# Kernel tuning notes

Hardware: AMD Instinct MI355X
Metric: run time of the kernel (lower is better)

## Reference

```python
import jax, jax.numpy as jnp
import numpy as np

N = 50000      # nodes
E = 800000     # edges
IN = 128       # in_dim
H = 128        # hidden_dim
OUT = 64       # out_dim
B = 6          # block_num
NEG_SLOPE = 0.01  # nn.LeakyReLU default


def setup_inputs() -> dict:
    key = jax.random.key(0)
    ks = jax.random.split(key, 10)
    s = 0.05
    return {
        "inputs": jax.random.normal(ks[0], (N, IN), jnp.float32),
        "edges": jax.random.randint(ks[1], (2, E), 0, N, jnp.int32),
        "w_in": jax.random.normal(ks[2], (IN, H), jnp.float32) * s,
        "b_in": jnp.zeros((H,), jnp.float32),
        "w1": jax.random.normal(ks[3], (B, H, H), jnp.float32) * s,
        "b1": jnp.zeros((B, H), jnp.float32),
        "w2": jax.random.normal(ks[4], (B, H, H), jnp.float32) * s,
        "b2": jnp.zeros((B, H), jnp.float32),
        "w_out": jax.random.normal(ks[5], (H, OUT), jnp.float32) * s,
        "b_out": jnp.zeros((OUT,), jnp.float32),
    }


def _leaky(x):
    return jnp.where(x >= 0, x, NEG_SLOPE * x)


def _gcn_conv(x, W, b, src, dst, norm):
    # GCNConv: out = D^{-1/2}(A+I)D^{-1/2} (x W) + b, with self-loops folded in.
    xw = x @ W                                   # [N, d_out]
    msg = xw[src] * norm[src, None]              # gather + edge scaling [E, d_out]
    agg = jax.ops.segment_sum(msg, dst, num_segments=N)
    agg = agg * norm[:, None] + xw * (norm * norm)[:, None]  # neighbors + self-loop
    return agg + b


def reference(inputs, edges, w_in, b_in, w1, b1, w2, b2, w_out, b_out):
    src, dst = edges[0], edges[1]
    deg = 1.0 + jax.ops.segment_sum(jnp.ones((E,), inputs.dtype), dst, num_segments=N)
    norm = jax.lax.rsqrt(deg)                    # [N]

    x = _leaky(_gcn_conv(inputs, w_in, b_in, src, dst, norm))
    for i in range(B):  # fixed small layer loop (structurally distinct params)
        h = _leaky(_gcn_conv(x, w1[i], b1[i], src, dst, norm))
        h = _leaky(_gcn_conv(h, w2[i], b2[i], src, dst, norm))
        x = (x + h) * 0.5
    # dropout in eval mode -> identity
    x_out = _gcn_conv(x, w_out, b_out, src, dst, norm)
    return (x_out, x)
```

## Files before the change

kernel.cpp:

```cpp
#include <hip/hip_runtime.h>

#define NNODES 50000
#define NPAD   50048
#define NEDGES 800000
#define HDIM 128
#define OUTDIM 64

#define GEMM_GRID 196
#define GEMM_BLK  512
#define GEMM_WAVES (GEMM_GRID * (GEMM_BLK / 64))
#define GEMM_TILES (NPAD / 16)

typedef short short8 __attribute__((ext_vector_type(8)));
typedef _Float16 half8 __attribute__((ext_vector_type(8)));
typedef _Float16 half4 __attribute__((ext_vector_type(4)));
typedef float f32x4 __attribute__((ext_vector_type(4)));

__device__ __forceinline__ unsigned short f2bf(float f) {
    unsigned int u = __builtin_bit_cast(unsigned int, f);
    unsigned int r = (u + 0x7FFFu + ((u >> 16) & 1u)) >> 16;
    return (unsigned short)r;
}
__device__ __forceinline__ float bf2f(unsigned short b) {
    unsigned int u = ((unsigned int)b) << 16;
    return __builtin_bit_cast(float, u);
}

__global__ void count_kernel(const int* __restrict__ dst, int* __restrict__ deg,
                             int* __restrict__ epos) {
    int e = blockIdx.x * 256 + threadIdx.x;
    if (e < NEDGES) epos[e] = atomicAdd(&deg[dst[e]], 1);
}

__global__ __launch_bounds__(256) void bsum_kernel(const int* __restrict__ deg,
                                                   int* __restrict__ bsum) {
    __shared__ int red[256];
    int i = blockIdx.x * 256 + threadIdx.x;
    red[threadIdx.x] = (i < NNODES) ? deg[i] : 0;
    __syncthreads();
    for (int off = 128; off; off >>= 1) {
        if (threadIdx.x < off) red[threadIdx.x] += red[threadIdx.x + off];
        __syncthreads();
    }
    if (threadIdx.x == 0) bsum[blockIdx.x] = red[0];
}

__global__ __launch_bounds__(256) void bscan_kernel(const int* __restrict__ bsum,
                                                    int* __restrict__ bofs) {
    __shared__ int s[256];
    int t = threadIdx.x;
    int v = (t < 196) ? bsum[t] : 0;
    s[t] = v;
    __syncthreads();
    for (int off = 1; off < 256; off <<= 1) {
        int u = (t >= off) ? s[t - off] : 0;
        __syncthreads();
        s[t] += u;
        __syncthreads();
    }
    if (t < 196) bofs[t] = s[t] - v;
}

__global__ __launch_bounds__(256) void emit_kernel(
    const int* __restrict__ deg, const int* __restrict__ bofs,
    int* __restrict__ row_ptr, float* __restrict__ norm) {
    __shared__ int s[256];
    int t = threadIdx.x;
    int i = blockIdx.x * 256 + t;
    int v = (i < NNODES) ? deg[i] : 0;
    s[t] = v;
    __syncthreads();
    for (int off = 1; off < 256; off <<= 1) {
        int u = (t >= off) ? s[t - off] : 0;
        __syncthreads();
        s[t] += u;
        __syncthreads();
    }
    int excl = s[t] - v + bofs[blockIdx.x];
    if (i < NNODES) {
        row_ptr[i] = excl;
        norm[i] = rsqrtf(1.0f + (float)v);
    }
    if (i == NNODES - 1) row_ptr[NNODES] = NEDGES;
}

__global__ void fill_kernel(const int* __restrict__ src, const int* __restrict__ dst,
                            const int* __restrict__ epos, const int* __restrict__ row_ptr,
                            int* __restrict__ sorted_src) {
    int e = blockIdx.x * 256 + threadIdx.x;
    if (e < NEDGES) sorted_src[row_ptr[dst[e]] + epos[e]] = src[e];
}

__global__ __launch_bounds__(256) void prep_w_kernel(
    const float* __restrict__ w_in, const float* __restrict__ w1,
    const float* __restrict__ w2, const float* __restrict__ w_out,
    unsigned short* __restrict__ wT, _Float16* __restrict__ w2f) {
    int idx = blockIdx.x * 256 + threadIdx.x;
    if (idx < 16384 + 98304) {
        const float* W;
        unsigned short* o;
        int e;
        if (idx < 16384) {
            W = w_in; o = wT; e = idx;
        } else {
            int j = idx - 16384; int m = j >> 14; e = j & 16383;
            W = w1 + ((size_t)m << 14); o = wT + (size_t)(1 + m) * 32768;
        }
        int k = e >> 7, n = e & 127;
        float v = W[e];
        unsigned short h = f2bf(v);
        o[(size_t)n * 256 + k] = h;
        o[(size_t)n * 256 + 128 + k] = f2bf(v - bf2f(h));
    } else if (idx < 16384 + 196608) {
        int j = idx - 16384 - 98304; int m = j >> 14; int e = j & 16383;
        int k = e >> 7, n = e & 127;
        w2f[(size_t)m * 16384 + n * 128 + k] = (_Float16)w2[((size_t)m << 14) + e];
    } else {
        int e = idx - 212992;
        int k = e >> 6, n = e & 63;
        float v = w_out[e];
        unsigned short h = f2bf(v);
        unsigned short* o = wT + (size_t)7 * 32768;
        o[(size_t)n * 256 + k] = h;
        o[(size_t)n * 256 + 128 + k] = f2bf(v - bf2f(h));
    }
}

__global__ __launch_bounds__(256) void split_x_kernel(
    const float* __restrict__ x, unsigned short* __restrict__ xc) {
    int gid = blockIdx.x * 256 + threadIdx.x;
    int row = gid >> 6;
    int kk = (gid & 63) * 2;
    float2 v = {0.f, 0.f};
    if (row < NNODES) v = *(const float2*)(x + (size_t)row * 128 + kk);
    unsigned short h0 = f2bf(v.x), h1 = f2bf(v.y);
    unsigned short l0 = f2bf(v.x - bf2f(h0)), l1 = f2bf(v.y - bf2f(h1));
    *(unsigned int*)(xc + (size_t)row * 256 + kk) =
        (unsigned int)h0 | ((unsigned int)h1 << 16);
    *(unsigned int*)(xc + (size_t)row * 256 + 128 + kk) =
        (unsigned int)l0 | ((unsigned int)l1 << 16);
}

template <int NCOLS>
__global__ __launch_bounds__(GEMM_BLK) void gemm_bf_kernel(
    const unsigned short* __restrict__ xc, const unsigned short* __restrict__ wT,
    const float* __restrict__ norm, _Float16* __restrict__ y) {
    __shared__ unsigned short Blds[NCOLS * 256];
    const int t = threadIdx.x;
    const int wave = t >> 6, lane = t & 63, quad = lane >> 4, l16 = lane & 15;

    constexpr int NCH = NCOLS * 32;
#pragma unroll
    for (int i = 0; i < NCH / GEMM_BLK; ++i) {
        int C = i * GEMM_BLK + t;
        int n = C >> 5, c = C & 31;
        const unsigned short* gp = wT + ((size_t)n << 8) + ((c ^ (n & 7)) << 3);
        unsigned short* lp = Blds + ((size_t)C << 3);
        __builtin_amdgcn_global_load_lds(
            (const __attribute__((address_space(1))) void*)gp,
            (__attribute__((address_space(3))) void*)lp, 16, 0, 0);
    }
    __syncthreads();

    const int wid = blockIdx.x * (GEMM_BLK / 64) + wave;
    const int sw = l16 & 7;
    const bool has1 = (wid + GEMM_WAVES) < GEMM_TILES;
    const int rb0 = wid * 16;
    const int rb1 = has1 ? (wid + GEMM_WAVES) * 16 : 0;

    short8 a0[8], a1[8];
    const unsigned short* ap0 = xc + ((size_t)(rb0 + l16) << 8) + quad * 8;
    const unsigned short* ap1 = xc + ((size_t)(rb1 + l16) << 8) + quad * 8;
#pragma unroll
    for (int ck = 0; ck < 8; ++ck) a0[ck] = *(const short8*)(ap0 + ck * 32);
#pragma unroll
    for (int ck = 0; ck < 8; ++ck) a1[ck] = *(const short8*)(ap1 + ck * 32);

    float nm0[4], nm1[4];
#pragma unroll
    for (int r = 0; r < 4; ++r) {
        int r0 = rb0 + quad * 4 + r;
        int r1 = rb1 + quad * 4 + r;
        nm0[r] = norm[r0 < NNODES ? r0 : 0];
        nm1[r] = norm[r1 < NNODES ? r1 : 0];
    }

#pragma unroll
    for (int nt = 0; nt < NCOLS / 16; ++nt) {
        const unsigned short* bp = Blds + ((size_t)(nt * 16 + l16) << 8);
        short8 bh[4], bl[4];
#pragma unroll
        for (int ck = 0; ck < 4; ++ck) {
            bh[ck] = *(const short8*)(bp + (((ck * 4 + quad) ^ sw) << 3));
            bl[ck] = *(const short8*)(bp + (((16 + ck * 4 + quad) ^ sw) << 3));
        }
        f32x4 ac0 = (f32x4){0.f, 0.f, 0.f, 0.f};
        f32x4 ac1 = (f32x4){0.f, 0.f, 0.f, 0.f};
#pragma unroll
        for (int ck = 0; ck < 4; ++ck) {
            ac0 = __builtin_amdgcn_mfma_f32_16x16x32_bf16(a0[ck], bh[ck], ac0, 0, 0, 0);
            ac1 = __builtin_amdgcn_mfma_f32_16x16x32_bf16(a1[ck], bh[ck], ac1, 0, 0, 0);
            ac0 = __builtin_amdgcn_mfma_f32_16x16x32_bf16(a0[ck], bl[ck], ac0, 0, 0, 0);
            ac1 = __builtin_amdgcn_mfma_f32_16x16x32_bf16(a1[ck], bl[ck], ac1, 0, 0, 0);
            ac0 = __builtin_amdgcn_mfma_f32_16x16x32_bf16(a0[4 + ck], bh[ck], ac0, 0, 0, 0);
            ac1 = __builtin_amdgcn_mfma_f32_16x16x32_bf16(a1[4 + ck], bh[ck], ac1, 0, 0, 0);
        }
        int col = nt * 16 + l16;
#pragma unroll
        for (int r = 0; r < 4; ++r) {
            int r0 = rb0 + quad * 4 + r;
            if (r0 < NNODES) y[(size_t)r0 * NCOLS + col] = (_Float16)(ac0[r] * nm0[r]);
            int r1 = rb1 + quad * 4 + r;
            if (has1 && r1 < NNODES) y[(size_t)r1 * NCOLS + col] = (_Float16)(ac1[r] * nm1[r]);
        }
    }
}

__global__ __launch_bounds__(GEMM_BLK) void gemm_f16_kernel(
    const _Float16* __restrict__ A, const _Float16* __restrict__ wf,
    const float* __restrict__ norm, _Float16* __restrict__ y) {
    __shared__ _Float16 Blds[128 * 128];
    const int t = threadIdx.x;
    const int wave = t >> 6, lane = t & 63, quad = lane >> 4, l16 = lane & 15;

#pragma unroll
    for (int i = 0; i < 2048 / GEMM_BLK; ++i) {
        int C = i * GEMM_BLK + t;
        int n = C >> 4, c = C & 15;
        const _Float16* gp = wf + ((size_t)n << 7) + ((c ^ (n & 7)) << 3);
        _Float16* lp = Blds + ((size_t)C << 3);
        __builtin_amdgcn_global_load_lds(
            (const __attribute__((address_space(1))) void*)gp,
            (__attribute__((address_space(3))) void*)lp, 16, 0, 0);
    }
    __syncthreads();

    const int wid = blockIdx.x * (GEMM_BLK / 64) + wave;
    const int sw = l16 & 7;
    const bool has1 = (wid + GEMM_WAVES) < GEMM_TILES;
    const int rb0 = wid * 16;
    const int rb1 = has1 ? (wid + GEMM_WAVES) * 16 : 0;

    half8 a0[4], a1[4];
    const _Float16* ap0 = A + ((size_t)(rb0 + l16) << 7) + quad * 8;
    const _Float16* ap1 = A + ((size_t)(rb1 + l16) << 7) + quad * 8;
#pragma unroll
    for (int ck = 0; ck < 4; ++ck) a0[ck] = *(const half8*)(ap0 + ck * 32);
#pragma unroll
    for (int ck = 0; ck < 4; ++ck) a1[ck] = *(const half8*)(ap1 + ck * 32);

    float nm0[4], nm1[4];
#pragma unroll
    for (int r = 0; r < 4; ++r) {
        int r0 = rb0 + quad * 4 + r;
        int r1 = rb1 + quad * 4 + r;
        nm0[r] = norm[r0 < NNODES ? r0 : 0];
        nm1[r] = norm[r1 < NNODES ? r1 : 0];
    }

#pragma unroll
    for (int nt = 0; nt < 8; ++nt) {
        const _Float16* bp = Blds + ((size_t)(nt * 16 + l16) << 7);
        half8 b[4];
#pragma unroll
        for (int ck = 0; ck < 4; ++ck)
            b[ck] = *(const half8*)(bp + (((ck * 4 + quad) ^ sw) << 3));
        f32x4 ac0 = (f32x4){0.f, 0.f, 0.f, 0.f};
        f32x4 ac1 = (f32x4){0.f, 0.f, 0.f, 0.f};
#pragma unroll
        for (int ck = 0; ck < 4; ++ck) {
            ac0 = __builtin_amdgcn_mfma_f32_16x16x32_f16(a0[ck], b[ck], ac0, 0, 0, 0);
            ac1 = __builtin_amdgcn_mfma_f32_16x16x32_f16(a1[ck], b[ck], ac1, 0, 0, 0);
        }
        int col = nt * 16 + l16;
#pragma unroll
        for (int r = 0; r < 4; ++r) {
            int r0 = rb0 + quad * 4 + r;
            if (r0 < NNODES) y[(size_t)r0 * 128 + col] = (_Float16)(ac0[r] * nm0[r]);
            int r1 = rb1 + quad * 4 + r;
            if (has1 && r1 < NNODES) y[(size_t)r1 * 128 + col] = (_Float16)(ac1[r] * nm1[r]);
        }
    }
}

template <int MODE, bool WOUT, bool OUT16>
__global__ __launch_bounds__(256) void gather_fin128(
    const _Float16* __restrict__ y, const int* __restrict__ row_ptr,
    const int* __restrict__ sorted_src, const float* __restrict__ norm,
    const float* __restrict__ bias, const unsigned short* __restrict__ xcres,
    float* __restrict__ out, unsigned short* __restrict__ xcout,
    _Float16* __restrict__ h16) {
    const int wave = threadIdx.x >> 6;
    const int lane = threadIdx.x & 63;
    const int g = lane >> 4, j = lane & 15;
    const int n = blockIdx.x * 16 + wave * 4 + g;
    const int beg = row_ptr[n];
    const int deg = row_ptr[n + 1] - beg;
    int dmax = deg;
    dmax = max(dmax, __shfl_xor(dmax, 16));
    dmax = max(dmax, __shfl_xor(dmax, 32));

    float acc[8];
#pragma unroll
    for (int c = 0; c < 8; ++c) acc[c] = 0.f;

    for (int i = 0; i < dmax; i += 8) {
        int sarr[8];
#pragma unroll
        for (int u = 0; u < 8; ++u)
            sarr[u] = (i + u < deg) ? sorted_src[beg + i + u] : -1;
        half8 h[8];
#pragma unroll
        for (int u = 0; u < 8; ++u)
            if (sarr[u] >= 0)
                h[u] = *(const half8*)(y + ((size_t)sarr[u] << 7) + j * 8);
#pragma unroll
        for (int u = 0; u < 8; ++u)
            if (sarr[u] >= 0) {
#pragma unroll
                for (int c = 0; c < 8; ++c) acc[c] += (float)h[u][c];
            }
    }

    const half8 sh = *(const half8*)(y + ((size_t)n << 7) + j * 8);
    const float4 b0 = *(const float4*)(bias + j * 8);
    const float4 b1 = *(const float4*)(bias + j * 8 + 4);
    const float bb[8] = {b0.x, b0.y, b0.z, b0.w, b1.x, b1.y, b1.z, b1.w};
    const float nm = norm[n];
    float v[8];
#pragma unroll
    for (int c = 0; c < 8; ++c) {
        float t = (acc[c] + (float)sh[c]) * nm + bb[c];
        v[c] = t >= 0.f ? t : 0.01f * t;
    }
    if (MODE == 1) {
        short8 hw = *(const short8*)(xcres + ((size_t)n << 8) + j * 8);
        short8 lw = *(const short8*)(xcres + ((size_t)n << 8) + 128 + j * 8);
#pragma unroll
        for (int c = 0; c < 8; ++c) {
            float xr = bf2f((unsigned short)hw[c]) + bf2f((unsigned short)lw[c]);
            v[c] = (xr + v[c]) * 0.5f;
        }
    }
    if (WOUT) {
        float4 o0 = {v[0], v[1], v[2], v[3]};
        float4 o1 = {v[4], v[5], v[6], v[7]};
        *(float4*)(out + ((size_t)n << 7) + j * 8) = o0;
        *(float4*)(out + ((size_t)n << 7) + j * 8 + 4) = o1;
    }
    if (OUT16) {
        half8 o;
#pragma unroll
        for (int c = 0; c < 8; ++c) o[c] = (_Float16)v[c];
        *(half8*)(h16 + ((size_t)n << 7) + j * 8) = o;
    } else {
        short8 hi, lo;
#pragma unroll
        for (int c = 0; c < 8; ++c) {
            unsigned short hv = f2bf(v[c]);
            hi[c] = (short)hv;
            lo[c] = (short)f2bf(v[c] - bf2f(hv));
        }
        *(short8*)(xcout + ((size_t)n << 8) + j * 8) = hi;
        *(short8*)(xcout + ((size_t)n << 8) + 128 + j * 8) = lo;
    }
}

__global__ __launch_bounds__(256) void gather_fin64(
    const _Float16* __restrict__ y, const int* __restrict__ row_ptr,
    const int* __restrict__ sorted_src, const float* __restrict__ norm,
    const float* __restrict__ bias, float* __restrict__ out) {
    const int wave = threadIdx.x >> 6;
    const int lane = threadIdx.x & 63;
    const int g = lane >> 4, j = lane & 15;
    const int n = blockIdx.x * 16 + wave * 4 + g;
    const int beg = row_ptr[n];
    const int deg = row_ptr[n + 1] - beg;
    int dmax = deg;
    dmax = max(dmax, __shfl_xor(dmax, 16));
    dmax = max(dmax, __shfl_xor(dmax, 32));

    float acc[4] = {0.f, 0.f, 0.f, 0.f};
    for (int i = 0; i < dmax; i += 8) {
        int sarr[8];
#pragma unroll
        for (int u = 0; u < 8; ++u)
            sarr[u] = (i + u < deg) ? sorted_src[beg + i + u] : -1;
        half4 h[8];
#pragma unroll
        for (int u = 0; u < 8; ++u)
            if (sarr[u] >= 0)
                h[u] = *(const half4*)(y + ((size_t)sarr[u] << 6) + j * 4);
#pragma unroll
        for (int u = 0; u < 8; ++u)
            if (sarr[u] >= 0) {
#pragma unroll
                for (int c = 0; c < 4; ++c) acc[c] += (float)h[u][c];
            }
    }

    const half4 sh = *(const half4*)(y + ((size_t)n << 6) + j * 4);
    const float4 b = *(const float4*)(bias + j * 4);
    const float bb[4] = {b.x, b.y, b.z, b.w};
    const float nm = norm[n];
    float4 o;
    o.x = (acc[0] + (float)sh[0]) * nm + bb[0];
    o.y = (acc[1] + (float)sh[1]) * nm + bb[1];
    o.z = (acc[2] + (float)sh[2]) * nm + bb[2];
    o.w = (acc[3] + (float)sh[3]) * nm + bb[3];
    *(float4*)(out + ((size_t)n << 6) + j * 4) = o;
}

extern "C" void kernel_launch(void* const* d_in, const int* in_sizes, int n_in,
                              void* d_out, int out_size, void* d_ws, size_t ws_size,
                              hipStream_t stream) {
    const float* inputs = (const float*)d_in[0];
    const int* edges = (const int*)d_in[1];
    const int* src = edges;
    const int* dst = edges + NEDGES;
    const float* w_in  = (const float*)d_in[2];
    const float* b_in  = (const float*)d_in[3];
    const float* w1    = (const float*)d_in[4];
    const float* b1    = (const float*)d_in[5];
    const float* w2    = (const float*)d_in[6];
    const float* b2    = (const float*)d_in[7];
    const float* w_out = (const float*)d_in[8];
    const float* b_out = (const float*)d_in[9];

    float* out  = (float*)d_out;
    float* xout = out;
    float* x    = out + (size_t)NNODES * OUTDIM;

    char* p = (char*)d_ws;
    auto alloc = [&](size_t bytes) {
        char* r = p;
        p += (bytes + 63) & ~(size_t)63;
        return r;
    };
    int* deg        = (int*)alloc(NNODES * 4);
    int* epos       = (int*)alloc(NEDGES * 4);
    int* row_ptr    = (int*)alloc((NNODES + 1) * 4);
    int* bsum       = (int*)alloc(256 * 4);
    int* bofs       = (int*)alloc(256 * 4);
    int* sorted_src = (int*)alloc(NEDGES * 4);
    float* normb    = (float*)alloc(NNODES * 4);
    unsigned short* wT = (unsigned short*)alloc((size_t)245760 * 2);
    _Float16* w2f   = (_Float16*)alloc((size_t)6 * 16384 * 2);
    unsigned short* xc_x = (unsigned short*)alloc((size_t)NPAD * 256 * 2);
    unsigned short* xc_in = (unsigned short*)alloc((size_t)NPAD * 256 * 2);
    _Float16* h16   = (_Float16*)alloc((size_t)NPAD * 128 * 2);
    _Float16* y     = (_Float16*)alloc((size_t)NNODES * HDIM * 2);

    hipMemsetAsync(deg, 0, NNODES * sizeof(int), stream);
    count_kernel<<<(NEDGES + 255) / 256, 256, 0, stream>>>(dst, deg, epos);
    bsum_kernel<<<196, 256, 0, stream>>>(deg, bsum);
    bscan_kernel<<<1, 256, 0, stream>>>(bsum, bofs);
    emit_kernel<<<196, 256, 0, stream>>>(deg, bofs, row_ptr, normb);
    fill_kernel<<<(NEDGES + 255) / 256, 256, 0, stream>>>(src, dst, epos, row_ptr, sorted_src);
    prep_w_kernel<<<864, 256, 0, stream>>>(w_in, w1, w2, w_out, wT, w2f);

    split_x_kernel<<<(NPAD * 64) / 256, 256, 0, stream>>>(inputs, xc_in);
    gemm_bf_kernel<128><<<GEMM_GRID, GEMM_BLK, 0, stream>>>(xc_in, wT, normb, y);
    gather_fin128<0, false, false><<<NNODES / 16, 256, 0, stream>>>(
        y, row_ptr, sorted_src, normb, b_in, nullptr, nullptr, xc_x, nullptr);

    for (int i = 0; i < 6; ++i) {
        gemm_bf_kernel<128><<<GEMM_GRID, GEMM_BLK, 0, stream>>>(
            xc_x, wT + (size_t)(1 + i) * 32768, normb, y);
        gather_fin128<0, false, true><<<NNODES / 16, 256, 0, stream>>>(
            y, row_ptr, sorted_src, normb, b1 + i * HDIM, nullptr, nullptr, nullptr, h16);
        gemm_f16_kernel<<<GEMM_GRID, GEMM_BLK, 0, stream>>>(
            h16, w2f + (size_t)i * 16384, normb, y);
        if (i < 5)
            gather_fin128<1, false, false><<<NNODES / 16, 256, 0, stream>>>(
                y, row_ptr, sorted_src, normb, b2 + i * HDIM, xc_x, nullptr, xc_x, nullptr);
        else
            gather_fin128<1, true, false><<<NNODES / 16, 256, 0, stream>>>(
                y, row_ptr, sorted_src, normb, b2 + i * HDIM, xc_x, x, xc_x, nullptr);
    }

    gemm_bf_kernel<64><<<GEMM_GRID, GEMM_BLK, 0, stream>>>(
        xc_x, wT + (size_t)7 * 32768, normb, y);
    gather_fin64<<<NNODES / 16, 256, 0, stream>>>(
        y, row_ptr, sorted_src, normb, b_out, xout);
}
```

Before: 788.1 us.

## Sort nodes by degree for gathers and use one row tile per GEMM wave

New measurement: 1.207 ms. 1.53x slower.

```diff
diff --git a/kernel.cpp b/kernel.cpp
--- a/kernel.cpp
+++ b/kernel.cpp
@@ -6,15 +6,17 @@
 #define HDIM 128
 #define OUTDIM 64
 
-#define GEMM_GRID 196
+#define GEMM_GRID 391
 #define GEMM_BLK  512
-#define GEMM_WAVES (GEMM_GRID * (GEMM_BLK / 64))
 #define GEMM_TILES (NPAD / 16)
+
+#define DBUCKETS 512
 
 typedef short short8 __attribute__((ext_vector_type(8)));
 typedef _Float16 half8 __attribute__((ext_vector_type(8)));
 typedef _Float16 half4 __attribute__((ext_vector_type(4)));
 typedef float f32x4 __attribute__((ext_vector_type(4)));
+typedef float f32x8 __attribute__((ext_vector_type(8)));
 
 __device__ __forceinline__ unsigned short f2bf(float f) {
     unsigned int u = __builtin_bit_cast(unsigned int, f);
@@ -89,6 +91,37 @@
                             int* __restrict__ sorted_src) {
     int e = blockIdx.x * 256 + threadIdx.x;
     if (e < NEDGES) sorted_src[row_ptr[dst[e]] + epos[e]] = src[e];
+}
+
+__global__ void dhist_kernel(const int* __restrict__ deg, int* __restrict__ dcount) {
+    int i = blockIdx.x * 256 + threadIdx.x;
+    if (i < NNODES) atomicAdd(&dcount[min(deg[i], DBUCKETS - 1)], 1);
+}
+
+__global__ __launch_bounds__(DBUCKETS) void dscan_kernel(const int* __restrict__ dcount,
+                                                         int* __restrict__ dofs) {
+    __shared__ int s[DBUCKETS];
+    int t = threadIdx.x;
+    int v = dcount[t];
+    s[t] = v;
+    __syncthreads();
+    for (int off = 1; off < DBUCKETS; off <<= 1) {
+        int u = (t >= off) ? s[t - off] : 0;
+        __syncthreads();
+        s[t] += u;
+        __syncthreads();
+    }
+    dofs[t] = s[t] - v;
+}
+
+__global__ void dscatter_kernel(const int* __restrict__ deg, int* __restrict__ dfill,
+                                const int* __restrict__ dofs, int* __restrict__ perm) {
+    int i = blockIdx.x * 256 + threadIdx.x;
+    if (i < NNODES) {
+        int b = min(deg[i], DBUCKETS - 1);
+        int pos = dofs[b] + atomicAdd(&dfill[b], 1);
+        perm[pos] = i;
+    }
 }
 
 __global__ __launch_bounds__(256) void prep_w_kernel(
@@ -164,25 +197,18 @@
 
     const int wid = blockIdx.x * (GEMM_BLK / 64) + wave;
     const int sw = l16 & 7;
-    const bool has1 = (wid + GEMM_WAVES) < GEMM_TILES;
     const int rb0 = wid * 16;
-    const int rb1 = has1 ? (wid + GEMM_WAVES) * 16 : 0;
-
-    short8 a0[8], a1[8];
+
+    short8 a0[8];
     const unsigned short* ap0 = xc + ((size_t)(rb0 + l16) << 8) + quad * 8;
-    const unsigned short* ap1 = xc + ((size_t)(rb1 + l16) << 8) + quad * 8;
 #pragma unroll
     for (int ck = 0; ck < 8; ++ck) a0[ck] = *(const short8*)(ap0 + ck * 32);
-#pragma unroll
-    for (int ck = 0; ck < 8; ++ck) a1[ck] = *(const short8*)(ap1 + ck * 32);
-
-    float nm0[4], nm1[4];
+
+    float nm0[4];
 #pragma unroll
     for (int r = 0; r < 4; ++r) {
         int r0 = rb0 + quad * 4 + r;
-        int r1 = rb1 + quad * 4 + r;
         nm0[r] = norm[r0 < NNODES ? r0 : 0];
-        nm1[r] = norm[r1 < NNODES ? r1 : 0];
     }
 
 #pragma unroll
@@ -195,23 +221,17 @@
             bl[ck] = *(const short8*)(bp + (((16 + ck * 4 + quad) ^ sw) << 3));
         }
         f32x4 ac0 = (f32x4){0.f, 0.f, 0.f, 0.f};
-        f32x4 ac1 = (f32x4){0.f, 0.f, 0.f, 0.f};
 #pragma unroll
         for (int ck = 0; ck < 4; ++ck) {
             ac0 = __builtin_amdgcn_mfma_f32_16x16x32_bf16(a0[ck], bh[ck], ac0, 0, 0, 0);
-            ac1 = __builtin_amdgcn_mfma_f32_16x16x32_bf16(a1[ck], bh[ck], ac1, 0, 0, 0);
             ac0 = __builtin_amdgcn_mfma_f32_16x16x32_bf16(a0[ck], bl[ck], ac0, 0, 0, 0);
-            ac1 = __builtin_amdgcn_mfma_f32_16x16x32_bf16(a1[ck], bl[ck], ac1, 0, 0, 0);
             ac0 = __builtin_amdgcn_mfma_f32_16x16x32_bf16(a0[4 + ck], bh[ck], ac0, 0, 0, 0);
-            ac1 = __builtin_amdgcn_mfma_f32_16x16x32_bf16(a1[4 + ck], bh[ck], ac1, 0, 0, 0);
         }
         int col = nt * 16 + l16;
 #pragma unroll
         for (int r = 0; r < 4; ++r) {
             int r0 = rb0 + quad * 4 + r;
             if (r0 < NNODES) y[(size_t)r0 * NCOLS + col] = (_Float16)(ac0[r] * nm0[r]);
-            int r1 = rb1 + quad * 4 + r;
-            if (has1 && r1 < NNODES) y[(size_t)r1 * NCOLS + col] = (_Float16)(ac1[r] * nm1[r]);
         }
     }
 }
@@ -237,25 +257,18 @@
 
     const int wid = blockIdx.x * (GEMM_BLK / 64) + wave;
     const int sw = l16 & 7;
-    const bool has1 = (wid + GEMM_WAVES) < GEMM_TILES;
     const int rb0 = wid * 16;
-    const int rb1 = has1 ? (wid + GEMM_WAVES) * 16 : 0;
-
-    half8 a0[4], a1[4];
+
+    half8 a0[4];
     const _Float16* ap0 = A + ((size_t)(rb0 + l16) << 7) + quad * 8;
-    const _Float16* ap1 = A + ((size_t)(rb1 + l16) << 7) + quad * 8;
 #pragma unroll
     for (int ck = 0; ck < 4; ++ck) a0[ck] = *(const half8*)(ap0 + ck * 32);
-#pragma unroll
-    for (int ck = 0; ck < 4; ++ck) a1[ck] = *(const half8*)(ap1 + ck * 32);
-
-    float nm0[4], nm1[4];
+
+    float nm0[4];
 #pragma unroll
     for (int r = 0; r < 4; ++r) {
         int r0 = rb0 + quad * 4 + r;
-        int r1 = rb1 + quad * 4 + r;
         nm0[r] = norm[r0 < NNODES ? r0 : 0];
-        nm1[r] = norm[r1 < NNODES ? r1 : 0];
     }
 
 #pragma unroll
@@ -266,19 +279,14 @@
         for (int ck = 0; ck < 4; ++ck)
             b[ck] = *(const half8*)(bp + (((ck * 4 + quad) ^ sw) << 3));
         f32x4 ac0 = (f32x4){0.f, 0.f, 0.f, 0.f};
-        f32x4 ac1 = (f32x4){0.f, 0.f, 0.f, 0.f};
-#pragma unroll
-        for (int ck = 0; ck < 4; ++ck) {
+#pragma unroll
+        for (int ck = 0; ck < 4; ++ck)
             ac0 = __builtin_amdgcn_mfma_f32_16x16x32_f16(a0[ck], b[ck], ac0, 0, 0, 0);
-            ac1 = __builtin_amdgcn_mfma_f32_16x16x32_f16(a1[ck], b[ck], ac1, 0, 0, 0);
-        }
         int col = nt * 16 + l16;
 #pragma unroll
         for (int r = 0; r < 4; ++r) {
             int r0 = rb0 + quad * 4 + r;
             if (r0 < NNODES) y[(size_t)r0 * 128 + col] = (_Float16)(ac0[r] * nm0[r]);
-            int r1 = rb1 + quad * 4 + r;
-            if (has1 && r1 < NNODES) y[(size_t)r1 * 128 + col] = (_Float16)(ac1[r] * nm1[r]);
         }
     }
 }
@@ -289,20 +297,18 @@
     const int* __restrict__ sorted_src, const float* __restrict__ norm,
     const float* __restrict__ bias, const unsigned short* __restrict__ xcres,
     float* __restrict__ out, unsigned short* __restrict__ xcout,
-    _Float16* __restrict__ h16) {
+    _Float16* __restrict__ h16, const int* __restrict__ perm) {
     const int wave = threadIdx.x >> 6;
     const int lane = threadIdx.x & 63;
     const int g = lane >> 4, j = lane & 15;
-    const int n = blockIdx.x * 16 + wave * 4 + g;
+    const int n = perm[blockIdx.x * 16 + wave * 4 + g];
     const int beg = row_ptr[n];
     const int deg = row_ptr[n + 1] - beg;
     int dmax = deg;
     dmax = max(dmax, __shfl_xor(dmax, 16));
     dmax = max(dmax, __shfl_xor(dmax, 32));
 
-    float acc[8];
-#pragma unroll
-    for (int c = 0; c < 8; ++c) acc[c] = 0.f;
+    f32x8 acc = (f32x8){0.f, 0.f, 0.f, 0.f, 0.f, 0.f, 0.f, 0.f};
 
     for (int i = 0; i < dmax; i += 8) {
         int sarr[8];
@@ -316,10 +322,7 @@
                 h[u] = *(const half8*)(y + ((size_t)sarr[u] << 7) + j * 8);
 #pragma unroll
         for (int u = 0; u < 8; ++u)
-            if (sarr[u] >= 0) {
-#pragma unroll
-                for (int c = 0; c < 8; ++c) acc[c] += (float)h[u][c];
-            }
+            if (sarr[u] >= 0) acc += __builtin_convertvector(h[u], f32x8);
     }
 
     const half8 sh = *(const half8*)(y + ((size_t)n << 7) + j * 8);
@@ -369,18 +372,19 @@
 __global__ __launch_bounds__(256) void gather_fin64(
     const _Float16* __restrict__ y, const int* __restrict__ row_ptr,
     const int* __restrict__ sorted_src, const float* __restrict__ norm,
-    const float* __restrict__ bias, float* __restrict__ out) {
+    const float* __restrict__ bias, float* __restrict__ out,
+    const int* __restrict__ perm) {
     const int wave = threadIdx.x >> 6;
     const int lane = threadIdx.x & 63;
     const int g = lane >> 4, j = lane & 15;
-    const int n = blockIdx.x * 16 + wave * 4 + g;
+    const int n = perm[blockIdx.x * 16 + wave * 4 + g];
     const int beg = row_ptr[n];
     const int deg = row_ptr[n + 1] - beg;
     int dmax = deg;
     dmax = max(dmax, __shfl_xor(dmax, 16));
     dmax = max(dmax, __shfl_xor(dmax, 32));
 
-    float acc[4] = {0.f, 0.f, 0.f, 0.f};
+    f32x4 acc = (f32x4){0.f, 0.f, 0.f, 0.f};
     for (int i = 0; i < dmax; i += 8) {
         int sarr[8];
 #pragma unroll
@@ -393,10 +397,7 @@
                 h[u] = *(const half4*)(y + ((size_t)sarr[u] << 6) + j * 4);
 #pragma unroll
         for (int u = 0; u < 8; ++u)
-            if (sarr[u] >= 0) {
-#pragma unroll
-                for (int c = 0; c < 4; ++c) acc[c] += (float)h[u][c];
-            }
+            if (sarr[u] >= 0) acc += __builtin_convertvector(h[u], f32x4);
     }
 
     const half4 sh = *(const half4*)(y + ((size_t)n << 6) + j * 4);
@@ -444,6 +445,9 @@
     int* bofs       = (int*)alloc(256 * 4);
     int* sorted_src = (int*)alloc(NEDGES * 4);
     float* normb    = (float*)alloc(NNODES * 4);
+    int* dctr       = (int*)alloc(2 * DBUCKETS * 4);
+    int* dofs       = (int*)alloc(DBUCKETS * 4);
+    int* perm       = (int*)alloc(NNODES * 4);
     unsigned short* wT = (unsigned short*)alloc((size_t)245760 * 2);
     _Float16* w2f   = (_Float16*)alloc((size_t)6 * 16384 * 2);
     unsigned short* xc_x = (unsigned short*)alloc((size_t)NPAD * 256 * 2);
@@ -451,8 +455,15 @@
     _Float16* h16   = (_Float16*)alloc((size_t)NPAD * 128 * 2);
     _Float16* y     = (_Float16*)alloc((size_t)NNODES * HDIM * 2);
 
+    int* dcount = dctr;
+    int* dfill  = dctr + DBUCKETS;
+
     hipMemsetAsync(deg, 0, NNODES * sizeof(int), stream);
+    hipMemsetAsync(dctr, 0, 2 * DBUCKETS * sizeof(int), stream);
     count_kernel<<<(NEDGES + 255) / 256, 256, 0, stream>>>(dst, deg, epos);
+    dhist_kernel<<<(NNODES + 255) / 256, 256, 0, stream>>>(deg, dcount);
+    dscan_kernel<<<1, DBUCKETS, 0, stream>>>(dcount, dofs);
+    dscatter_kernel<<<(NNODES + 255) / 256, 256, 0, stream>>>(deg, dfill, dofs, perm);
     bsum_kernel<<<196, 256, 0, stream>>>(deg, bsum);
     bscan_kernel<<<1, 256, 0, stream>>>(bsum, bofs);
     emit_kernel<<<196, 256, 0, stream>>>(deg, bofs, row_ptr, normb);
@@ -462,25 +473,25 @@
     split_x_kernel<<<(NPAD * 64) / 256, 256, 0, stream>>>(inputs, xc_in);
     gemm_bf_kernel<128><<<GEMM_GRID, GEMM_BLK, 0, stream>>>(xc_in, wT, normb, y);
     gather_fin128<0, false, false><<<NNODES / 16, 256, 0, stream>>>(
-        y, row_ptr, sorted_src, normb, b_in, nullptr, nullptr, xc_x, nullptr);
+        y, row_ptr, sorted_src, normb, b_in, nullptr, nullptr, xc_x, nullptr, perm);
 
     for (int i = 0; i < 6; ++i) {
         gemm_bf_kernel<128><<<GEMM_GRID, GEMM_BLK, 0, stream>>>(
             xc_x, wT + (size_t)(1 + i) * 32768, normb, y);
         gather_fin128<0, false, true><<<NNODES / 16, 256, 0, stream>>>(
-            y, row_ptr, sorted_src, normb, b1 + i * HDIM, nullptr, nullptr, nullptr, h16);
+            y, row_ptr, sorted_src, normb, b1 + i * HDIM, nullptr, nullptr, nullptr, h16, perm);
         gemm_f16_kernel<<<GEMM_GRID, GEMM_BLK, 0, stream>>>(
             h16, w2f + (size_t)i * 16384, normb, y);
         if (i < 5)
             gather_fin128<1, false, false><<<NNODES / 16, 256, 0, stream>>>(
-                y, row_ptr, sorted_src, normb, b2 + i * HDIM, xc_x, nullptr, xc_x, nullptr);
+                y, row_ptr, sorted_src, normb, b2 + i * HDIM, xc_x, nullptr, xc_x, nullptr, perm);
         else
             gather_fin128<1, true, false><<<NNODES / 16, 256, 0, stream>>>(
-                y, row_ptr, sorted_src, normb, b2 + i * HDIM, xc_x, x, xc_x, nullptr);
+                y, row_ptr, sorted_src, normb, b2 + i * HDIM, xc_x, x, xc_x, nullptr, perm);
     }
 
     gemm_bf_kernel<64><<<GEMM_GRID, GEMM_BLK, 0, stream>>>(
         xc_x, wT + (size_t)7 * 32768, normb, y);
     gather_fin64<<<NNODES / 16, 256, 0, stream>>>(
-        y, row_ptr, sorted_src, normb, b_out, xout);
-}
+        y, row_ptr, sorted_src, normb, b_out, xout, perm);
+}
```
